# Kernel tuning notes

Measured on AMD Instinct MI355X. Metric: run time of the kernel, lower is better.

The kernel has to match this reference:

```python
import jax, jax.numpy as jnp
import numpy as np

S = 14        # grid size
B = 2         # boxes per cell
NC = 20       # classes
N = 4096      # batch
L_COORD = 5.0
L_NOOBJ = 0.5


def _xywh2xyxy(b):
    # b[..., :2] are cell-center coords (scaled by 1/S), b[..., 2:4] are w,h
    xy = b[..., :2] / S
    wh = b[..., 2:4]
    return jnp.concatenate([xy - 0.5 * wh, xy + 0.5 * wh], axis=-1)


def _iou(b1, b2):
    # elementwise (broadcasting) IoU over last dim [x1,y1,x2,y2]
    lt = jnp.maximum(b1[..., :2], b2[..., :2])
    rb = jnp.minimum(b1[..., 2:4], b2[..., 2:4])
    wh = jnp.clip(rb - lt, 0.0)
    inter = wh[..., 0] * wh[..., 1]
    a1 = (b1[..., 2] - b1[..., 0]) * (b1[..., 3] - b1[..., 1])
    a2 = (b2[..., 2] - b2[..., 0]) * (b2[..., 3] - b2[..., 1])
    return inter / (a1 + a2 - inter)


def setup_inputs() -> dict:
    key = jax.random.key(0)
    k1, k2, k3, k4 = jax.random.split(key, 4)
    pred_tensor = jax.random.uniform(k1, (N, S, S, B * 5 + NC), dtype=jnp.float32)
    target_boxes = jax.random.uniform(k2, (N, S, S, 4), dtype=jnp.float32)
    target_cls = jax.random.uniform(k3, (N, S, S, NC), dtype=jnp.float32)
    has_object_map = jax.random.bernoulli(k4, 0.15, (N, S, S))
    return dict(pred_tensor=pred_tensor, target_boxes=target_boxes,
                target_cls=target_cls, has_object_map=has_object_map)


def reference(pred_tensor, target_boxes, target_cls, has_object_map):
    n = pred_tensor.shape[0]
    pb = pred_tensor[..., :B * 5].reshape(n, S, S, B, 5)   # (N,S,S,B,5)
    pcls = pred_tensor[..., B * 5:]                        # (N,S,S,20)
    m = has_object_map                                     # (N,S,S) bool
    mf = m.astype(pred_tensor.dtype)

    # class loss: masked sum of squares over object cells
    cls_loss = jnp.sum(jnp.where(m[..., None], (pcls - target_cls) ** 2, 0.0))

    # no-object loss: confidence^2 summed over non-object cells, both boxes
    noobj_loss = jnp.sum(jnp.where(~m[..., None], pb[..., 4] ** 2, 0.0))

    # best-iou box selection (iou is treated as ground truth: no gradient)
    iou = _iou(_xywh2xyxy(pb[..., :4]),
               _xywh2xyxy(target_boxes)[..., None, :])    # (N,S,S,B)
    iou = jax.lax.stop_gradient(iou)
    best = jnp.argmax(iou, axis=-1)                        # (N,S,S)
    best_iou = jnp.max(iou, axis=-1)                       # (N,S,S)
    resp = jnp.take_along_axis(pb, best[..., None, None], axis=3)[..., 0, :]  # (N,S,S,5)

    reg_loss = (jnp.sum(mf[..., None] * (resp[..., :2] - target_boxes[..., :2]) ** 2)
                + jnp.sum(mf[..., None] * (jnp.sqrt(resp[..., 2:4])
                                           - jnp.sqrt(target_boxes[..., 2:4])) ** 2))

    # containing-object confidence loss vs best iou (target detached)
    contain_loss = jnp.sum(mf * (resp[..., 4] - best_iou) ** 2)

    total = (L_COORD * reg_loss + L_NOOBJ * noobj_loss + contain_loss + cls_loss) / n
    return jnp.stack([total, reg_loss, contain_loss, noobj_loss, cls_loss])
```

## Files before the change

### kernel.cpp

```cpp
#include <hip/hip_runtime.h>


#define GS 14
#define NCLS 20
#define BLOCK 256
#define NSLOTS 64
#define SLOT_STRIDE 16
#define WAVE_F 1920
#define SLAB_F (4 * WAVE_F)


__device__ __forceinline__ void gload_lds16(const float* g, float* l) {
    __builtin_amdgcn_global_load_lds(
        (const __attribute__((address_space(1))) void*)g,
        (__attribute__((address_space(3))) void*)l, 16, 0, 0);
}
__device__ __forceinline__ void gload_lds4(const float* g, float* l) {
    __builtin_amdgcn_global_load_lds(
        (const __attribute__((address_space(1))) void*)g,
        (__attribute__((address_space(3))) void*)l, 4, 0, 0);
}

__device__ __forceinline__ void cell_compute(const float (&v)[30],
                                             const float4 tb4,
                                             const float* __restrict__ tcls,
                                             int cell, bool m,
                                             float& reg, float& cont,
                                             float& noobj, float& cls) {
    const float invS = 1.0f / (float)GS;
    if (m) {
        const float tx = tb4.x, ty = tb4.y, tw = tb4.z, th = tb4.w;

        const float tcx = tx * invS, tcy = ty * invS;
        const float t_x1 = tcx - 0.5f * tw, t_y1 = tcy - 0.5f * th;
        const float t_x2 = tcx + 0.5f * tw, t_y2 = tcy + 0.5f * th;
        const float ta = (t_x2 - t_x1) * (t_y2 - t_y1);

        const float b0x = v[0], b0y = v[1], b0w = v[2], b0h = v[3], b0c = v[4];
        const float b1x = v[5], b1y = v[6], b1w = v[7], b1h = v[8], b1c = v[9];

        float iou0, iou1;
        {
            const float cx = b0x * invS, cy = b0y * invS;
            const float x1 = cx - 0.5f * b0w, y1 = cy - 0.5f * b0h;
            const float x2 = cx + 0.5f * b0w, y2 = cy + 0.5f * b0h;
            const float iw = fmaxf(fminf(x2, t_x2) - fmaxf(x1, t_x1), 0.0f);
            const float ih = fmaxf(fminf(y2, t_y2) - fmaxf(y1, t_y1), 0.0f);
            const float inter = iw * ih;
            const float pa = (x2 - x1) * (y2 - y1);
            iou0 = inter / (pa + ta - inter);
        }
        {
            const float cx = b1x * invS, cy = b1y * invS;
            const float x1 = cx - 0.5f * b1w, y1 = cy - 0.5f * b1h;
            const float x2 = cx + 0.5f * b1w, y2 = cy + 0.5f * b1h;
            const float iw = fmaxf(fminf(x2, t_x2) - fmaxf(x1, t_x1), 0.0f);
            const float ih = fmaxf(fminf(y2, t_y2) - fmaxf(y1, t_y1), 0.0f);
            const float inter = iw * ih;
            const float pa = (x2 - x1) * (y2 - y1);
            iou1 = inter / (pa + ta - inter);
        }

        const bool sel1 = iou1 > iou0;
        const float biou = fmaxf(iou0, iou1);
        const float rx = sel1 ? b1x : b0x;
        const float ry = sel1 ? b1y : b0y;
        const float rw = sel1 ? b1w : b0w;
        const float rh = sel1 ? b1h : b0h;
        const float rc = sel1 ? b1c : b0c;

        const float d0 = rx - tx, d1 = ry - ty;
        const float d2 = sqrtf(rw) - sqrtf(tw);
        const float d3 = sqrtf(rh) - sqrtf(th);
        reg += d0 * d0 + d1 * d1 + d2 * d2 + d3 * d3;

        const float dc = rc - biou;
        cont += dc * dc;

        const float4* tc4 = reinterpret_cast<const float4*>(tcls + (size_t)cell * NCLS);
        float csum = 0.0f;
        #pragma unroll
        for (int j = 0; j < 5; ++j) {
            const float4 t4 = tc4[j];
            float d;
            d = v[10 + j * 4 + 0] - t4.x; csum += d * d;
            d = v[10 + j * 4 + 1] - t4.y; csum += d * d;
            d = v[10 + j * 4 + 2] - t4.z; csum += d * d;
            d = v[10 + j * 4 + 3] - t4.w; csum += d * d;
        }
        cls += csum;
    } else {
        const float c0 = v[4], c1 = v[9];
        noobj += c0 * c0 + c1 * c1;
    }
}

__launch_bounds__(BLOCK)
__global__ void yolo_loss_kernel(const float* __restrict__ pred,
                                 const float* __restrict__ tbox,
                                 const float* __restrict__ tcls,
                                 const void* __restrict__ mask,
                                 float* __restrict__ ws,
                                 int ncells) {
    __shared__ float slab[SLAB_F];
    const int tid = threadIdx.x;
    const int wv = tid >> 6;
    const int lane = tid & 63;

    int my_bits = 0;
    if (ncells >= 4096) {
        const uint4 w4 = reinterpret_cast<const uint4*>(mask)[tid];
        const unsigned a = w4.x | w4.y | w4.z | w4.w;
        my_bits  = ((a & 0xFEFEFEFEu) != 0) ? 2 : 0;
        my_bits |= ((a & 0xFFFFFF00u) != 0) ? 1 : 0;
    } else if (tid == 0) {
        const unsigned char* mb = (const unsigned char*)mask;
        for (int i = 0; i < ncells; ++i) {
            if (mb[i] > 1) my_bits |= 2;
            if ((i & 3) != 0 && mb[i] != 0) my_bits |= 1;
        }
    }
    const int bits = __syncthreads_or(my_bits);
    const int fmt = (bits & 2) ? 2 : ((bits & 1) ? 1 : 0);

    const int base = blockIdx.x * BLOCK;
    const int cell = base + tid;

    float reg = 0.0f, cont = 0.0f, noobj = 0.0f, cls = 0.0f;

    if (base + BLOCK <= ncells) {
        const float* gsrc = pred + (size_t)blockIdx.x * SLAB_F + wv * WAVE_F;
        float* ldst = slab + wv * WAVE_F;
        #pragma unroll
        for (int i = 0; i < 7; ++i)
            gload_lds16(gsrc + i * 256 + lane * 4, ldst + i * 256);
        #pragma unroll
        for (int k = 0; k < 2; ++k)
            gload_lds4(gsrc + 1792 + k * 64 + lane, ldst + 1792 + k * 64);

        bool m;
        if (fmt == 2)      m = ((const float*)mask)[cell] != 0.0f;
        else if (fmt == 1) m = ((const unsigned char*)mask)[cell] != 0;
        else               m = ((const int*)mask)[cell] != 0;
        const float4 tb4 = reinterpret_cast<const float4*>(tbox)[cell];

        asm volatile("s_waitcnt vmcnt(0)" ::: "memory");
        __builtin_amdgcn_sched_barrier(0);

        float v[30];
        const float* lrow = slab + wv * WAVE_F + lane * 30;
        #pragma unroll
        for (int j = 0; j < 7; ++j)
            *reinterpret_cast<float4*>(&v[j * 4]) =
                *reinterpret_cast<const float4*>(lrow + j * 4);
        *reinterpret_cast<float2*>(&v[28]) =
            *reinterpret_cast<const float2*>(lrow + 28);

        cell_compute(v, tb4, tcls, cell, m, reg, cont, noobj, cls);
    } else if (cell < ncells) {
        bool m;
        if (fmt == 2)      m = ((const float*)mask)[cell] != 0.0f;
        else if (fmt == 1) m = ((const unsigned char*)mask)[cell] != 0;
        else               m = ((const int*)mask)[cell] != 0;
        float v[30];
        #pragma unroll
        for (int f = 0; f < 30; ++f) v[f] = pred[(size_t)cell * 30 + f];
        float4 tb;
        tb.x = tbox[(size_t)cell * 4 + 0];
        tb.y = tbox[(size_t)cell * 4 + 1];
        tb.z = tbox[(size_t)cell * 4 + 2];
        tb.w = tbox[(size_t)cell * 4 + 3];
        cell_compute(v, tb, tcls, cell, m, reg, cont, noobj, cls);
    }

    #pragma unroll
    for (int off = 32; off > 0; off >>= 1) {
        reg   += __shfl_down(reg, off);
        cont  += __shfl_down(cont, off);
        noobj += __shfl_down(noobj, off);
        cls   += __shfl_down(cls, off);
    }

    __shared__ float sred[4][4];
    if (lane == 0) {
        sred[wv][0] = reg; sred[wv][1] = cont;
        sred[wv][2] = noobj; sred[wv][3] = cls;
    }
    __syncthreads();
    if (tid == 0) {
        float r = 0, c = 0, no = 0, cl = 0;
        #pragma unroll
        for (int w = 0; w < 4; ++w) {
            r += sred[w][0]; c += sred[w][1]; no += sred[w][2]; cl += sred[w][3];
        }
        float* slot = ws + (size_t)(blockIdx.x & (NSLOTS - 1)) * SLOT_STRIDE;
        atomicAdd(&slot[0], r);
        atomicAdd(&slot[1], c);
        atomicAdd(&slot[2], no);
        atomicAdd(&slot[3], cl);
    }
}

__global__ void yolo_finalize_kernel(const float* __restrict__ ws,
                                     float* __restrict__ out, float inv_n) {
    const int t = threadIdx.x;
    float reg   = ws[t * SLOT_STRIDE + 0];
    float cont  = ws[t * SLOT_STRIDE + 1];
    float noobj = ws[t * SLOT_STRIDE + 2];
    float cls   = ws[t * SLOT_STRIDE + 3];
    #pragma unroll
    for (int off = 32; off > 0; off >>= 1) {
        reg   += __shfl_down(reg, off);
        cont  += __shfl_down(cont, off);
        noobj += __shfl_down(noobj, off);
        cls   += __shfl_down(cls, off);
    }
    if (t == 0) {
        const float total = (5.0f * reg + 0.5f * noobj + cont + cls) * inv_n;
        out[0] = total;
        out[1] = reg;
        out[2] = cont;
        out[3] = noobj;
        out[4] = cls;
    }
}

extern "C" void kernel_launch(void* const* d_in, const int* in_sizes, int n_in,
                              void* d_out, int out_size, void* d_ws, size_t ws_size,
                              hipStream_t stream) {
    const float* pred = (const float*)d_in[0];
    const float* tbox = (const float*)d_in[1];
    const float* tcls = (const float*)d_in[2];
    const void*  mask = d_in[3];
    float* ws  = (float*)d_ws;
    float* out = (float*)d_out;

    const int ncells = in_sizes[3];
    const int n_img  = ncells / (GS * GS);
    const float inv_n = 1.0f / (float)n_img;

    hipMemsetAsync(ws, 0, NSLOTS * SLOT_STRIDE * sizeof(float), stream);

    const int grid = (ncells + BLOCK - 1) / BLOCK;
    yolo_loss_kernel<<<grid, BLOCK, 0, stream>>>(pred, tbox, tcls, mask, ws, ncells);

    yolo_finalize_kernel<<<1, 64, 0, stream>>>(ws, out, inv_n);
}
```

Baseline: 33.47 us.

## Process two cells per thread with overlapped LDS staging of second slab

Each block now handles 512 cells instead of 256. After the first slab's rows are read from LDS, each wave issues the global-to-LDS copy for the second slab and runs the first cell's compute while that load is in flight. This halves the grid and the per-block reduction and atomic work, and hides some load latency. The cost is fewer blocks for parallelism and serialization inside each wave. The tail path is turned into a strided loop.

```diff
diff --git a/kernel.cpp b/kernel.cpp
--- a/kernel.cpp
+++ b/kernel.cpp
@@ -4,6 +4,7 @@
 #define GS 14
 #define NCLS 20
 #define BLOCK 256
+#define CPB 512
 #define NSLOTS 64
 #define SLOT_STRIDE 16
 #define WAVE_F 1920
@@ -19,6 +20,15 @@
     __builtin_amdgcn_global_load_lds(
         (const __attribute__((address_space(1))) void*)g,
         (__attribute__((address_space(3))) void*)l, 4, 0, 0);
+}
+
+__device__ __forceinline__ void stage_wave(const float* gsrc, float* ldst, int lane) {
+    #pragma unroll
+    for (int i = 0; i < 7; ++i)
+        gload_lds16(gsrc + i * 256 + lane * 4, ldst + i * 256);
+    #pragma unroll
+    for (int k = 0; k < 2; ++k)
+        gload_lds4(gsrc + 1792 + k * 64 + lane, ldst + 1792 + k * 64);
 }
 
 __device__ __forceinline__ void cell_compute(const float (&v)[30],
@@ -93,6 +103,15 @@
         const float c0 = v[4], c1 = v[9];
         noobj += c0 * c0 + c1 * c1;
     }
+}
+
+__device__ __forceinline__ void ds_read_row(const float* lrow, float (&v)[30]) {
+    #pragma unroll
+    for (int j = 0; j < 7; ++j)
+        *reinterpret_cast<float4*>(&v[j * 4]) =
+            *reinterpret_cast<const float4*>(lrow + j * 4);
+    *reinterpret_cast<float2*>(&v[28]) =
+        *reinterpret_cast<const float2*>(lrow + 28);
 }
 
 __launch_bounds__(BLOCK)
@@ -123,54 +142,71 @@
     const int bits = __syncthreads_or(my_bits);
     const int fmt = (bits & 2) ? 2 : ((bits & 1) ? 1 : 0);
 
-    const int base = blockIdx.x * BLOCK;
-    const int cell = base + tid;
+    const int base = blockIdx.x * CPB;
 
     float reg = 0.0f, cont = 0.0f, noobj = 0.0f, cls = 0.0f;
 
-    if (base + BLOCK <= ncells) {
-        const float* gsrc = pred + (size_t)blockIdx.x * SLAB_F + wv * WAVE_F;
+    if (base + CPB <= ncells) {
+        const int cellA = base + wv * 64 + lane;
+        const int cellB = cellA + 256;
+
+        const float* gsrcA = pred + (size_t)(base + wv * 64) * 30;
+        const float* gsrcB = gsrcA + 256 * 30;
         float* ldst = slab + wv * WAVE_F;
-        #pragma unroll
-        for (int i = 0; i < 7; ++i)
-            gload_lds16(gsrc + i * 256 + lane * 4, ldst + i * 256);
-        #pragma unroll
-        for (int k = 0; k < 2; ++k)
-            gload_lds4(gsrc + 1792 + k * 64 + lane, ldst + 1792 + k * 64);
-
-        bool m;
-        if (fmt == 2)      m = ((const float*)mask)[cell] != 0.0f;
-        else if (fmt == 1) m = ((const unsigned char*)mask)[cell] != 0;
-        else               m = ((const int*)mask)[cell] != 0;
-        const float4 tb4 = reinterpret_cast<const float4*>(tbox)[cell];
+        const float* lrow = ldst + lane * 30;
+
+        stage_wave(gsrcA, ldst, lane);
+
+        bool mA, mB;
+        if (fmt == 2) {
+            mA = ((const float*)mask)[cellA] != 0.0f;
+            mB = ((const float*)mask)[cellB] != 0.0f;
+        } else if (fmt == 1) {
+            mA = ((const unsigned char*)mask)[cellA] != 0;
+            mB = ((const unsigned char*)mask)[cellB] != 0;
+        } else {
+            mA = ((const int*)mask)[cellA] != 0;
+            mB = ((const int*)mask)[cellB] != 0;
+        }
+        const float4 tbA = reinterpret_cast<const float4*>(tbox)[cellA];
+        const float4 tbB = reinterpret_cast<const float4*>(tbox)[cellB];
 
         asm volatile("s_waitcnt vmcnt(0)" ::: "memory");
         __builtin_amdgcn_sched_barrier(0);
 
-        float v[30];
-        const float* lrow = slab + wv * WAVE_F + lane * 30;
-        #pragma unroll
-        for (int j = 0; j < 7; ++j)
-            *reinterpret_cast<float4*>(&v[j * 4]) =
-                *reinterpret_cast<const float4*>(lrow + j * 4);
-        *reinterpret_cast<float2*>(&v[28]) =
-            *reinterpret_cast<const float2*>(lrow + 28);
-
-        cell_compute(v, tb4, tcls, cell, m, reg, cont, noobj, cls);
-    } else if (cell < ncells) {
-        bool m;
-        if (fmt == 2)      m = ((const float*)mask)[cell] != 0.0f;
-        else if (fmt == 1) m = ((const unsigned char*)mask)[cell] != 0;
-        else               m = ((const int*)mask)[cell] != 0;
-        float v[30];
-        #pragma unroll
-        for (int f = 0; f < 30; ++f) v[f] = pred[(size_t)cell * 30 + f];
-        float4 tb;
-        tb.x = tbox[(size_t)cell * 4 + 0];
-        tb.y = tbox[(size_t)cell * 4 + 1];
-        tb.z = tbox[(size_t)cell * 4 + 2];
-        tb.w = tbox[(size_t)cell * 4 + 3];
-        cell_compute(v, tb, tcls, cell, m, reg, cont, noobj, cls);
+        float vA[30];
+        ds_read_row(lrow, vA);
+
+        asm volatile("s_waitcnt lgkmcnt(0)" ::: "memory");
+        __builtin_amdgcn_sched_barrier(0);
+
+        stage_wave(gsrcB, ldst, lane);
+
+        cell_compute(vA, tbA, tcls, cellA, mA, reg, cont, noobj, cls);
+
+        asm volatile("s_waitcnt vmcnt(0)" ::: "memory");
+        __builtin_amdgcn_sched_barrier(0);
+
+        float vB[30];
+        ds_read_row(lrow, vB);
+
+        cell_compute(vB, tbB, tcls, cellB, mB, reg, cont, noobj, cls);
+    } else {
+        for (int cell = base + tid; cell < ncells; cell += BLOCK) {
+            bool m;
+            if (fmt == 2)      m = ((const float*)mask)[cell] != 0.0f;
+            else if (fmt == 1) m = ((const unsigned char*)mask)[cell] != 0;
+            else               m = ((const int*)mask)[cell] != 0;
+            float v[30];
+            #pragma unroll
+            for (int f = 0; f < 30; ++f) v[f] = pred[(size_t)cell * 30 + f];
+            float4 tb;
+            tb.x = tbox[(size_t)cell * 4 + 0];
+            tb.y = tbox[(size_t)cell * 4 + 1];
+            tb.z = tbox[(size_t)cell * 4 + 2];
+            tb.w = tbox[(size_t)cell * 4 + 3];
+            cell_compute(v, tb, tcls, cell, m, reg, cont, noobj, cls);
+        }
     }
 
     #pragma unroll
@@ -241,7 +277,7 @@
 
     hipMemsetAsync(ws, 0, NSLOTS * SLOT_STRIDE * sizeof(float), stream);
 
-    const int grid = (ncells + BLOCK - 1) / BLOCK;
+    const int grid = (ncells + CPB - 1) / CPB;
     yolo_loss_kernel<<<grid, BLOCK, 0, stream>>>(pred, tbox, tcls, mask, ws, ncells);
 
     yolo_finalize_kernel<<<1, 64, 0, stream>>>(ws, out, inv_n);
```

Measured after the change: 33.33 us. Within noise of the previous version (-0.4%).
